# Performance work log

Hardware: AMD Instinct MI355X
Metric: run time of the kernel (lower is better)

## Reference

```python
import jax, jax.numpy as jnp
import numpy as np

NUM_NEURONS = 10000
D = 784
BATCH = 4096


def setup_inputs() -> dict:
    key = jax.random.key(0)
    kx, kw = jax.random.split(key)
    x = jax.random.normal(kx, (BATCH, D), dtype=jnp.float32)
    weights = jax.random.normal(kw, (NUM_NEURONS, D), dtype=jnp.float32)
    return {"x": x, "weights": weights}


def reference(x, weights):
    # SOM BMU lookup: squared distances between each input row and every
    # codebook row, argmin over the codebook, gather the winning neuron.
    # Use |a|^2 + |b|^2 - 2ab to avoid the (B, N, D) broadcast intermediate.
    x = x.reshape(-1, D)  # (B, D)
    x_sq = jnp.sum(x * x, axis=1, keepdims=True)          # (B, 1)
    w_sq = jnp.sum(weights * weights, axis=1)             # (N,)
    cross = x @ weights.T                                 # (B, N) GEMM
    distances = x_sq + w_sq[None, :] - 2.0 * cross        # (B, N)
    bmu_indices = jnp.argmin(distances, axis=1)           # (B,)
    bmu = jnp.take(weights, bmu_indices, axis=0)          # (B, D)
    return bmu
```

## Files before the change

kernel.cpp:

```cpp
#include <hip/hip_runtime.h>
#include <math.h>

#define BATCH 4096
#define D 784
#define N 10000

#define KP 800
#define BK 32
#define KT (KP / BK)
#define BM 128
#define BN 128
#define GXMAX 80
#define NPAD (GXMAX * BN)
#define MARGIN 3.0f

typedef __attribute__((ext_vector_type(8))) short bh8;
typedef __attribute__((ext_vector_type(4))) float fx4;
typedef const __attribute__((address_space(1))) void CGV;
typedef __attribute__((address_space(3))) void LDSV;

static __device__ __forceinline__ unsigned short f2bf(float f) {
    unsigned u = __float_as_uint(f);
    unsigned r = u + 0x7fffu + ((u >> 16) & 1u);
    return (unsigned short)(r >> 16);
}

static __device__ __forceinline__ void top2_insert(float w, int j, float& v0, int& i0,
                                                   float& v1, int& i1) {
    if (w < v0 || (w == v0 && j < i0)) { v1 = v0; i1 = i0; v0 = w; i0 = j; }
    else if (w < v1 || (w == v1 && j < i1)) { v1 = w; i1 = j; }
}

__global__ __launch_bounds__(256) void convert_x_kernel(const float* __restrict__ x,
                                                        unsigned short* __restrict__ xh) {
    int row = blockIdx.x;
    const float4* xr = (const float4*)(x + (size_t)row * D);
    unsigned short* dst = xh + (size_t)row * KP;
    for (int i = threadIdx.x; i < KP / 4; i += 256) {
        int k = i * 4;
        uint2 o;
        if (k < D) {
            float4 v = xr[i];
            o.x = (unsigned)f2bf(v.x) | ((unsigned)f2bf(v.y) << 16);
            o.y = (unsigned)f2bf(v.z) | ((unsigned)f2bf(v.w) << 16);
        } else { o.x = 0u; o.y = 0u; }
        *(uint2*)(dst + k) = o;
    }
}

__global__ __launch_bounds__(256) void convert_w_kernel(const float* __restrict__ w,
                                                        unsigned short* __restrict__ wh,
                                                        float* __restrict__ wsq) {
    int row = blockIdx.x;
    unsigned short* dst = wh + (size_t)row * KP;
    float s = 0.f;
    if (row < N) {
        const float4* wr = (const float4*)(w + (size_t)row * D);
        for (int i = threadIdx.x; i < KP / 4; i += 256) {
            int k = i * 4;
            uint2 o;
            if (k < D) {
                float4 v = wr[i];
                s += v.x * v.x + v.y * v.y + v.z * v.z + v.w * v.w;
                o.x = (unsigned)f2bf(v.x) | ((unsigned)f2bf(v.y) << 16);
                o.y = (unsigned)f2bf(v.z) | ((unsigned)f2bf(v.w) << 16);
            } else { o.x = 0u; o.y = 0u; }
            *(uint2*)(dst + k) = o;
        }
    } else {
        for (int i = threadIdx.x; i < KP / 4; i += 256) {
            uint2 o; o.x = 0u; o.y = 0u;
            *(uint2*)(dst + i * 4) = o;
        }
    }
    __shared__ float sred[4];
    #pragma unroll
    for (int off = 32; off; off >>= 1) s += __shfl_down(s, off);
    if ((threadIdx.x & 63) == 0) sred[threadIdx.x >> 6] = s;
    __syncthreads();
    if (threadIdx.x == 0) {
        float t = sred[0] + sred[1] + sred[2] + sred[3];
        wsq[row] = (row < N) ? t : INFINITY;
    }
}

__global__ __launch_bounds__(256, 4) void dist_mfma_kernel(
    const unsigned short* __restrict__ xh, const unsigned short* __restrict__ wh,
    const float* __restrict__ wsq, float4* __restrict__ partial,
    int gx, int cpb) {
    __shared__ __align__(16) unsigned short As[2][BM * BK];
    __shared__ __align__(16) unsigned short Bs[2][BN * BK];
    __shared__ float4 red[BM][2];

    const int tid = threadIdx.x;
    const int lane = tid & 63;
    const int wid = tid >> 6;
    const int waveM = (wid >> 1) * 64;
    const int waveN = (wid & 1) * 64;

    const int L = blockIdx.x + gx * blockIdx.y;
    const int xcd = L & 7;
    const int s = L >> 3;
    const int bx = s >> 2;
    const int by = xcd * 4 + (s & 3);
    const int rowBase = by * BM;
    const int colBase0 = bx * (cpb * BN);

    const int rr = tid >> 2;
    const int csw = (tid & 3) ^ ((rr >> 1) & 3);
    const unsigned short* aSrc0 = xh + (size_t)(rowBase + rr) * KP + csw * 8;
    const unsigned short* aSrc1 = aSrc0 + (size_t)64 * KP;

    char* ldsA0 = (char*)&As[0][0] + wid * 1024;
    char* ldsA1 = (char*)&As[1][0] + wid * 1024;
    char* ldsB0 = (char*)&Bs[0][0] + wid * 1024;
    char* ldsB1 = (char*)&Bs[1][0] + wid * 1024;

    int offA[4], offB[4];
    #pragma unroll
    for (int m = 0; m < 4; m++) {
        int r = waveM + m * 16 + (lane & 15);
        offA[m] = r * BK + (((lane >> 4) ^ ((r >> 1) & 3)) << 3);
    }
    #pragma unroll
    for (int n = 0; n < 4; n++) {
        int r = waveN + n * 16 + (lane & 15);
        offB[n] = r * BK + (((lane >> 4) ^ ((r >> 1) & 3)) << 3);
    }

    float V0[16], V1[16];
    int I0[16], I1[16];
    #pragma unroll
    for (int q = 0; q < 16; q++) {
        V0[q] = INFINITY; V1[q] = INFINITY;
        I0[q] = 0x7fffffff; I1[q] = 0x7fffffff;
    }

#define STAGE(nb, k0)                                                                  \
    do {                                                                               \
        __builtin_amdgcn_global_load_lds((CGV*)(aSrc0 + (k0)), (LDSV*)(ldsA##nb), 16, 0, 0);        \
        __builtin_amdgcn_global_load_lds((CGV*)(aSrc1 + (k0)), (LDSV*)(ldsA##nb + 4096), 16, 0, 0); \
        __builtin_amdgcn_global_load_lds((CGV*)(bSrc0 + (k0)), (LDSV*)(ldsB##nb), 16, 0, 0);        \
        __builtin_amdgcn_global_load_lds((CGV*)(bSrc1 + (k0)), (LDSV*)(ldsB##nb + 4096), 16, 0, 0); \
    } while (0)

#define COMPUTE(nb)                                                                    \
    do {                                                                               \
        bh8 af[4], bf[4];                                                              \
        _Pragma("unroll")                                                              \
        for (int m = 0; m < 4; m++) af[m] = *(const bh8*)&As[nb][offA[m]];             \
        _Pragma("unroll")                                                              \
        for (int n = 0; n < 4; n++) bf[n] = *(const bh8*)&Bs[nb][offB[n]];             \
        _Pragma("unroll")                                                              \
        for (int m = 0; m < 4; m++)                                                    \
            _Pragma("unroll")                                                          \
            for (int n = 0; n < 4; n++)                                                \
                acc[m][n] = __builtin_amdgcn_mfma_f32_16x16x32_bf16(af[m], bf[n],      \
                                                                    acc[m][n], 0, 0, 0); \
    } while (0)

#define VM0 asm volatile("s_waitcnt vmcnt(0)" ::: "memory")
#define BARR __builtin_amdgcn_s_barrier()

    #pragma unroll 1
    for (int c = 0; c < cpb; ++c) {
        const int colBase = colBase0 + c * BN;
        const unsigned short* bSrc0 = wh + (size_t)(colBase + rr) * KP + csw * 8;
        const unsigned short* bSrc1 = bSrc0 + (size_t)64 * KP;

        fx4 acc[4][4];
        #pragma unroll
        for (int m = 0; m < 4; m++)
            #pragma unroll
            for (int n = 0; n < 4; n++) acc[m][n] = (fx4)0.f;

        STAGE(0, 0);
        VM0; BARR;
        #pragma unroll 1
        for (int t = 0; t < KT - 1; t += 2) {
            STAGE(1, (t + 1) * BK);
            COMPUTE(0);
            VM0; BARR;
            STAGE(0, (t + 2) * BK);
            COMPUTE(1);
            VM0; BARR;
        }
        COMPUTE(0);

        const int cb = colBase + waveN + (lane & 15);
        #pragma unroll
        for (int n = 0; n < 4; n++) {
            const float wq = wsq[cb + n * 16];
            const int ci = cb + n * 16;
            #pragma unroll
            for (int m = 0; m < 4; m++)
                #pragma unroll
                for (int r = 0; r < 4; r++) {
                    float dv = wq - 2.f * acc[m][n][r];
                    top2_insert(dv, ci, V0[m * 4 + r], I0[m * 4 + r],
                                V1[m * 4 + r], I1[m * 4 + r]);
                }
        }
        __syncthreads();
    }

#undef STAGE
#undef COMPUTE
#undef VM0
#undef BARR

    #pragma unroll
    for (int q = 0; q < 16; q++) {
        float v0 = V0[q], v1 = V1[q];
        int i0 = I0[q], i1 = I1[q];
        #pragma unroll
        for (int mask = 1; mask < 16; mask <<= 1) {
            float w0 = __shfl_xor(v0, mask); int j0 = __shfl_xor(i0, mask);
            float w1 = __shfl_xor(v1, mask); int j1 = __shfl_xor(i1, mask);
            top2_insert(w0, j0, v0, i0, v1, i1);
            top2_insert(w1, j1, v0, i0, v1, i1);
        }
        if ((lane & 15) == 0) {
            int m = q >> 2, r = q & 3;
            int row_local = waveM + m * 16 + (lane >> 4) * 4 + r;
            red[row_local][wid & 1] =
                make_float4(v0, __int_as_float(i0), v1, __int_as_float(i1));
        }
    }
    __syncthreads();
    if (tid < BM) {
        float4 pa = red[tid][0], pb = red[tid][1];
        float v0 = pa.x, v1 = pa.z;
        int i0 = __float_as_int(pa.y), i1 = __float_as_int(pa.w);
        top2_insert(pb.x, __float_as_int(pb.y), v0, i0, v1, i1);
        top2_insert(pb.z, __float_as_int(pb.w), v0, i0, v1, i1);
        partial[(size_t)(rowBase + tid) * gx + bx] =
            make_float4(v0, __int_as_float(i0), v1, __int_as_float(i1));
    }
}

__global__ __launch_bounds__(256) void rescore_kernel(const float* __restrict__ x,
                                                      const float* __restrict__ w,
                                                      const float4* __restrict__ partial,
                                                      float* __restrict__ out, int ng) {
    int wid = threadIdx.x >> 6, lane = threadIdx.x & 63;
    int row = blockIdx.x * 4 + wid;
    __shared__ int s_cnt[4];
    __shared__ int s_cand[4][64];

    const float4* part = partial + (size_t)row * ng;

    float bv = INFINITY;
    for (int c = lane; c < ng; c += 64) bv = fminf(bv, part[c].x);
    #pragma unroll
    for (int mask = 1; mask < 64; mask <<= 1) bv = fminf(bv, __shfl_xor(bv, mask));
    float thr = bv + MARGIN;

    if (lane == 0) s_cnt[wid] = 0;
    __syncthreads();
    for (int c = lane; c < ng; c += 64) {
        float4 p = part[c];
        if (p.x <= thr) {
            int pos = atomicAdd(&s_cnt[wid], 1);
            if (pos < 64) s_cand[wid][pos] = __float_as_int(p.y);
        }
        if (p.z <= thr) {
            int pos = atomicAdd(&s_cnt[wid], 1);
            if (pos < 64) s_cand[wid][pos] = __float_as_int(p.w);
        }
    }
    __syncthreads();
    int cnt = s_cnt[wid]; if (cnt > 64) cnt = 64;

    double bd = INFINITY; int bi = 0x7fffffff;
    for (int c = 0; c < cnt; c++) {
        int idx = s_cand[wid][c];
        const float* wr = w + (size_t)idx * D;
        const float* xr = x + (size_t)row * D;
        double s = 0.0;
        for (int d = lane; d < D; d += 64) {
            double wv = (double)wr[d];
            s += wv * (wv - 2.0 * (double)xr[d]);
        }
        #pragma unroll
        for (int mask = 1; mask < 64; mask <<= 1) s += __shfl_xor(s, mask);
        if (s < bd || (s == bd && idx < bi)) { bd = s; bi = idx; }
    }

    const float4* src = (const float4*)(w + (size_t)bi * D);
    float4* dst = (float4*)(out + (size_t)row * D);
    for (int i = lane; i < D / 4; i += 64) dst[i] = src[i];
}

extern "C" void kernel_launch(void* const* d_in, const int* in_sizes, int n_in,
                              void* d_out, int out_size, void* d_ws, size_t ws_size,
                              hipStream_t stream) {
    const float* x = (const float*)d_in[0];
    const float* w = (const float*)d_in[1];
    float* out = (float*)d_out;

    const size_t off_xh = 0;
    const size_t off_wh = off_xh + (size_t)BATCH * KP * 2;
    const size_t off_wsq = off_wh + (size_t)NPAD * KP * 2;
    const size_t off_part = off_wsq + (size_t)NPAD * 4;

    int gx = 80, cpb = 1;
    if (ws_size < off_part + (size_t)BATCH * 80 * 16) { gx = 40; cpb = 2; }
    if (ws_size < off_part + (size_t)BATCH * 40 * 16) { gx = 20; cpb = 4; }

    unsigned short* xh = (unsigned short*)((char*)d_ws + off_xh);
    unsigned short* wh = (unsigned short*)((char*)d_ws + off_wh);
    float* wsq = (float*)((char*)d_ws + off_wsq);
    float4* partial = (float4*)((char*)d_ws + off_part);

    hipLaunchKernelGGL(convert_x_kernel, dim3(BATCH), dim3(256), 0, stream, x, xh);
    hipLaunchKernelGGL(convert_w_kernel, dim3(NPAD), dim3(256), 0, stream, w, wh, wsq);
    hipLaunchKernelGGL(dist_mfma_kernel, dim3(gx, 32), dim3(256), 0, stream,
                       xh, wh, wsq, partial, gx, cpb);
    hipLaunchKernelGGL(rescore_kernel, dim3(BATCH / 4), dim3(256), 0, stream,
                       x, w, partial, out, gx);
}
```

Measured before the change: 570.8 us.

## Triple-buffer LDS tiles with partial vmcnt waits in GEMM main loop

Moves the A/B LDS staging from double to triple buffering. Loads are issued two K-steps ahead, and the loop waits with vmcnt(4) so the previous stage's loads can still be in flight. It also fully unrolls the K loop and cuts each iteration to one barrier instead of waiting on all loads before every compute. In exchange, LDS use rises and the occupancy hint drops from 4 to 3 blocks per CU, which lowers latency hiding across waves.

```diff
diff --git a/kernel.cpp b/kernel.cpp
--- a/kernel.cpp
+++ b/kernel.cpp
@@ -84,12 +84,12 @@
     }
 }
 
-__global__ __launch_bounds__(256, 4) void dist_mfma_kernel(
+__global__ __launch_bounds__(256, 3) void dist_mfma_kernel(
     const unsigned short* __restrict__ xh, const unsigned short* __restrict__ wh,
     const float* __restrict__ wsq, float4* __restrict__ partial,
     int gx, int cpb) {
-    __shared__ __align__(16) unsigned short As[2][BM * BK];
-    __shared__ __align__(16) unsigned short Bs[2][BN * BK];
+    __shared__ __align__(16) unsigned short As[3][BM * BK];
+    __shared__ __align__(16) unsigned short Bs[3][BN * BK];
     __shared__ float4 red[BM][2];
 
     const int tid = threadIdx.x;
@@ -111,21 +111,19 @@
     const unsigned short* aSrc0 = xh + (size_t)(rowBase + rr) * KP + csw * 8;
     const unsigned short* aSrc1 = aSrc0 + (size_t)64 * KP;
 
-    char* ldsA0 = (char*)&As[0][0] + wid * 1024;
-    char* ldsA1 = (char*)&As[1][0] + wid * 1024;
-    char* ldsB0 = (char*)&Bs[0][0] + wid * 1024;
-    char* ldsB1 = (char*)&Bs[1][0] + wid * 1024;
+    char* const ldsA = (char*)&As[0][0] + wid * 1024;
+    char* const ldsB = (char*)&Bs[0][0] + wid * 1024;
 
     int offA[4], offB[4];
     #pragma unroll
     for (int m = 0; m < 4; m++) {
         int r = waveM + m * 16 + (lane & 15);
-        offA[m] = r * BK + (((lane >> 4) ^ ((r >> 1) & 3)) << 3);
+        offA[m] = (r * BK + (((lane >> 4) ^ ((r >> 1) & 3)) << 3)) * 2;
     }
     #pragma unroll
     for (int n = 0; n < 4; n++) {
         int r = waveN + n * 16 + (lane & 15);
-        offB[n] = r * BK + (((lane >> 4) ^ ((r >> 1) & 3)) << 3);
+        offB[n] = (r * BK + (((lane >> 4) ^ ((r >> 1) & 3)) << 3)) * 2;
     }
 
     float V0[16], V1[16];
@@ -136,30 +134,33 @@
         I0[q] = 0x7fffffff; I1[q] = 0x7fffffff;
     }
 
-#define STAGE(nb, k0)                                                                  \
-    do {                                                                               \
-        __builtin_amdgcn_global_load_lds((CGV*)(aSrc0 + (k0)), (LDSV*)(ldsA##nb), 16, 0, 0);        \
-        __builtin_amdgcn_global_load_lds((CGV*)(aSrc1 + (k0)), (LDSV*)(ldsA##nb + 4096), 16, 0, 0); \
-        __builtin_amdgcn_global_load_lds((CGV*)(bSrc0 + (k0)), (LDSV*)(ldsB##nb), 16, 0, 0);        \
-        __builtin_amdgcn_global_load_lds((CGV*)(bSrc1 + (k0)), (LDSV*)(ldsB##nb + 4096), 16, 0, 0); \
+#define STAGE(buf, k0)                                                                     \
+    do {                                                                                   \
+        char* a_ = ldsA + (buf) * 8192;                                                    \
+        char* b_ = ldsB + (buf) * 8192;                                                    \
+        __builtin_amdgcn_global_load_lds((CGV*)(aSrc0 + (k0)), (LDSV*)a_, 16, 0, 0);       \
+        __builtin_amdgcn_global_load_lds((CGV*)(aSrc1 + (k0)), (LDSV*)(a_ + 4096), 16, 0, 0); \
+        __builtin_amdgcn_global_load_lds((CGV*)(bSrc0 + (k0)), (LDSV*)b_, 16, 0, 0);       \
+        __builtin_amdgcn_global_load_lds((CGV*)(bSrc1 + (k0)), (LDSV*)(b_ + 4096), 16, 0, 0); \
     } while (0)
 
-#define COMPUTE(nb)                                                                    \
-    do {                                                                               \
-        bh8 af[4], bf[4];                                                              \
-        _Pragma("unroll")                                                              \
-        for (int m = 0; m < 4; m++) af[m] = *(const bh8*)&As[nb][offA[m]];             \
-        _Pragma("unroll")                                                              \
-        for (int n = 0; n < 4; n++) bf[n] = *(const bh8*)&Bs[nb][offB[n]];             \
-        _Pragma("unroll")                                                              \
-        for (int m = 0; m < 4; m++)                                                    \
-            _Pragma("unroll")                                                          \
-            for (int n = 0; n < 4; n++)                                                \
-                acc[m][n] = __builtin_amdgcn_mfma_f32_16x16x32_bf16(af[m], bf[n],      \
-                                                                    acc[m][n], 0, 0, 0); \
+#define COMPUTE(buf)                                                                       \
+    do {                                                                                   \
+        const char* ab_ = (const char*)&As[0][0] + (buf) * 8192;                           \
+        const char* bb_ = (const char*)&Bs[0][0] + (buf) * 8192;                           \
+        bh8 af[4], bf[4];                                                                  \
+        _Pragma("unroll")                                                                  \
+        for (int m = 0; m < 4; m++) af[m] = *(const bh8*)(ab_ + offA[m]);                  \
+        _Pragma("unroll")                                                                  \
+        for (int n = 0; n < 4; n++) bf[n] = *(const bh8*)(bb_ + offB[n]);                  \
+        _Pragma("unroll")                                                                  \
+        for (int m = 0; m < 4; m++)                                                        \
+            _Pragma("unroll")                                                              \
+            for (int n = 0; n < 4; n++)                                                    \
+                acc[m][n] = __builtin_amdgcn_mfma_f32_16x16x32_bf16(af[m], bf[n],          \
+                                                                    acc[m][n], 0, 0, 0);   \
     } while (0)
 
-#define VM0 asm volatile("s_waitcnt vmcnt(0)" ::: "memory")
 #define BARR __builtin_amdgcn_s_barrier()
 
     #pragma unroll 1
@@ -175,17 +176,16 @@
             for (int n = 0; n < 4; n++) acc[m][n] = (fx4)0.f;
 
         STAGE(0, 0);
-        VM0; BARR;
-        #pragma unroll 1
-        for (int t = 0; t < KT - 1; t += 2) {
-            STAGE(1, (t + 1) * BK);
-            COMPUTE(0);
-            VM0; BARR;
-            STAGE(0, (t + 2) * BK);
-            COMPUTE(1);
-            VM0; BARR;
-        }
-        COMPUTE(0);
+        STAGE(1, BK);
+
+        #pragma unroll
+        for (int t = 0; t < KT; ++t) {
+            if (t < KT - 1) { asm volatile("s_waitcnt vmcnt(4)" ::: "memory"); }
+            else            { asm volatile("s_waitcnt vmcnt(0)" ::: "memory"); }
+            BARR;
+            if (t + 2 < KT) STAGE((t + 2) % 3, (t + 2) * BK);
+            COMPUTE(t % 3);
+        }
 
         const int cb = colBase + waveN + (lane & 15);
         #pragma unroll
@@ -206,7 +206,6 @@
 
 #undef STAGE
 #undef COMPUTE
-#undef VM0
 #undef BARR
 
     #pragma unroll
```

New measurement: 673.2 us. 1.18x slower.

## Add 256x256-tile 512-thread MFMA distance kernel with BK=64 staging

Applied to the files above, without the earlier changes.

Adds a new distance kernel that uses 256x256 output tiles, 8 waves and 128 KB of LDS, staging K in 64-wide chunks with an XOR-swizzled layout and a tail step for the last 32 columns. Each block does the top-2 reduction within each wave and then across waves in LDS. It writes one partial per 256-column tile, so the partial buffer and the rescore pass shrink to 40 candidates per row. The older kernel is kept as a fallback when the workspace is small, with a changed block remap. The larger tiles raise data reuse per LDS load but lower occupancy and grid size, and the kernel needs 128 KB of LDS per block.

```diff
diff --git a/kernel.cpp b/kernel.cpp
--- a/kernel.cpp
+++ b/kernel.cpp
@@ -6,13 +6,18 @@
 #define N 10000
 
 #define KP 800
-#define BK 32
-#define KT (KP / BK)
+#define NPAD 10240
+#define MARGIN 3.0f
+
+#define BM2 256
+#define BN2 256
+#define GX2 40
+#define GY2 16
+
 #define BM 128
 #define BN 128
-#define GXMAX 80
-#define NPAD (GXMAX * BN)
-#define MARGIN 3.0f
+#define BK 32
+#define KT 25
 
 typedef __attribute__((ext_vector_type(8))) short bh8;
 typedef __attribute__((ext_vector_type(4))) float fx4;
@@ -84,12 +89,154 @@
     }
 }
 
-__global__ __launch_bounds__(256, 4) void dist_mfma_kernel(
+__global__ __launch_bounds__(512, 2) void dist_mfma256_kernel(
+    const unsigned short* __restrict__ xh, const unsigned short* __restrict__ wh,
+    const float* __restrict__ wsq, float4* __restrict__ partial) {
+    __shared__ __align__(16) char smem[131072];
+
+    const int tid = threadIdx.x;
+    const int lane = tid & 63;
+    const int wid = tid >> 6;
+    const int waveM = (wid >> 2) * 128;
+    const int wn = wid & 3;
+    const int waveN = wn * 64;
+
+    const int L = blockIdx.x + GX2 * blockIdx.y;
+    const int xcd = L & 7;
+    const int sg = L >> 3;
+    const int bx = sg >> 1;
+    const int by = xcd * 2 + (sg & 1);
+    const int rowBase = by * BM2;
+    const int colBase = bx * BN2;
+
+    const int rr = tid >> 3;
+    const int ps = tid & 7;
+    const int ls = ps ^ (rr & 7);
+    const unsigned short* aS = xh + (size_t)(rowBase + rr) * KP + ls * 8;
+    const unsigned short* bS = wh + (size_t)(colBase + rr) * KP + ls * 8;
+    const int lsc = (ls < 4) ? ls : 3;
+    const unsigned short* aT = xh + (size_t)(rowBase + rr) * KP + 768 + lsc * 8;
+    const unsigned short* bT = wh + (size_t)(colBase + rr) * KP + 768 + lsc * 8;
+
+    char* const ldsA = smem + wid * 1024;
+    char* const ldsB = smem + 32768 + wid * 1024;
+
+    fx4 acc[8][4];
+    #pragma unroll
+    for (int m = 0; m < 8; m++)
+        #pragma unroll
+        for (int n = 0; n < 4; n++) acc[m][n] = (fx4)0.f;
+
+#define STAGE2(buf, k0, Asrc, Bsrc)                                                   \
+    do {                                                                              \
+        char* a_ = ldsA + (buf) * 65536;                                              \
+        char* b_ = ldsB + (buf) * 65536;                                              \
+        _Pragma("unroll")                                                             \
+        for (int j = 0; j < 4; j++) {                                                 \
+            __builtin_amdgcn_global_load_lds((CGV*)(Asrc + (k0) + (size_t)j * 64 * KP), \
+                                             (LDSV*)(a_ + j * 8192), 16, 0, 0);       \
+            __builtin_amdgcn_global_load_lds((CGV*)(Bsrc + (k0) + (size_t)j * 64 * KP), \
+                                             (LDSV*)(b_ + j * 8192), 16, 0, 0);       \
+        }                                                                             \
+    } while (0)
+
+#define KSUB(buf, s)                                                                  \
+    do {                                                                              \
+        const char* A_ = smem + (buf) * 65536;                                        \
+        const char* B_ = smem + (buf) * 65536 + 32768;                                \
+        bh8 af[8], bf[4];                                                             \
+        _Pragma("unroll")                                                             \
+        for (int m = 0; m < 8; m++) {                                                 \
+            int row = waveM + m * 16 + (lane & 15);                                   \
+            int seg = ((s) * 4 + (lane >> 4)) ^ (lane & 7);                           \
+            af[m] = *(const bh8*)(A_ + row * 128 + seg * 16);                         \
+        }                                                                             \
+        _Pragma("unroll")                                                             \
+        for (int n = 0; n < 4; n++) {                                                 \
+            int row = waveN + n * 16 + (lane & 15);                                   \
+            int seg = ((s) * 4 + (lane >> 4)) ^ (lane & 7);                           \
+            bf[n] = *(const bh8*)(B_ + row * 128 + seg * 16);                         \
+        }                                                                             \
+        _Pragma("unroll")                                                             \
+        for (int m = 0; m < 8; m++)                                                   \
+            _Pragma("unroll")                                                         \
+            for (int n = 0; n < 4; n++)                                               \
+                acc[m][n] = __builtin_amdgcn_mfma_f32_16x16x32_bf16(af[m], bf[n],     \
+                                                                    acc[m][n], 0, 0, 0); \
+    } while (0)
+
+    STAGE2(0, 0, aS, bS);
+    asm volatile("s_waitcnt vmcnt(0)" ::: "memory");
+    __builtin_amdgcn_s_barrier();
+
+    #pragma unroll
+    for (int t = 0; t < 12; ++t) {
+        if (t < 11) STAGE2((t + 1) & 1, (t + 1) * 64, aS, bS);
+        else        STAGE2(0, 0, aT, bT);
+        KSUB(t & 1, 0);
+        KSUB(t & 1, 1);
+        asm volatile("s_waitcnt vmcnt(0)" ::: "memory");
+        __builtin_amdgcn_s_barrier();
+    }
+    KSUB(0, 0);
+    __syncthreads();
+
+#undef STAGE2
+#undef KSUB
+
+    float4* red4 = (float4*)smem;
+    const int colT = colBase + waveN + (lane & 15);
+    float wq[4]; int ci[4];
+    #pragma unroll
+    for (int n = 0; n < 4; n++) { ci[n] = colT + n * 16; wq[n] = wsq[ci[n]]; }
+
+    #pragma unroll
+    for (int m = 0; m < 8; m++) {
+        #pragma unroll
+        for (int r = 0; r < 4; r++) {
+            float v0 = INFINITY, v1 = INFINITY;
+            int i0 = 0x7fffffff, i1 = 0x7fffffff;
+            #pragma unroll
+            for (int n = 0; n < 4; n++) {
+                float dv = wq[n] - 2.f * acc[m][n][r];
+                top2_insert(dv, ci[n], v0, i0, v1, i1);
+            }
+            #pragma unroll
+            for (int mask = 1; mask < 16; mask <<= 1) {
+                float w0 = __shfl_xor(v0, mask); int j0 = __shfl_xor(i0, mask);
+                float w1 = __shfl_xor(v1, mask); int j1 = __shfl_xor(i1, mask);
+                top2_insert(w0, j0, v0, i0, v1, i1);
+                top2_insert(w1, j1, v0, i0, v1, i1);
+            }
+            if ((lane & 15) == 0) {
+                int row_local = waveM + m * 16 + (lane >> 4) * 4 + r;
+                red4[row_local * 4 + wn] =
+                    make_float4(v0, __int_as_float(i0), v1, __int_as_float(i1));
+            }
+        }
+    }
+    __syncthreads();
+    if (tid < BM2) {
+        float4 p0 = red4[tid * 4 + 0];
+        float v0 = p0.x, v1 = p0.z;
+        int i0 = __float_as_int(p0.y), i1 = __float_as_int(p0.w);
+        #pragma unroll
+        for (int g = 1; g < 4; g++) {
+            float4 p = red4[tid * 4 + g];
+            top2_insert(p.x, __float_as_int(p.y), v0, i0, v1, i1);
+            top2_insert(p.z, __float_as_int(p.w), v0, i0, v1, i1);
+        }
+        partial[(size_t)(rowBase + tid) * GX2 + bx] =
+            make_float4(v0, __int_as_float(i0), v1, __int_as_float(i1));
+    }
+}
+
+__global__ __launch_bounds__(256, 2) void dist_r3_kernel(
     const unsigned short* __restrict__ xh, const unsigned short* __restrict__ wh,
     const float* __restrict__ wsq, float4* __restrict__ partial,
     int gx, int cpb) {
     __shared__ __align__(16) unsigned short As[2][BM * BK];
-    __shared__ __align__(16) unsigned short Bs[2][BN * BK];
+    __shared__ __align__(16) unsigned short Bs[2][BM * BK];
     __shared__ float4 red[BM][2];
 
     const int tid = threadIdx.x;
@@ -99,10 +246,9 @@
     const int waveN = (wid & 1) * 64;
 
     const int L = blockIdx.x + gx * blockIdx.y;
-    const int xcd = L & 7;
-    const int s = L >> 3;
-    const int bx = s >> 2;
-    const int by = xcd * 4 + (s & 3);
+    const int G = (L & 7) * (gx * 4) + (L >> 3);
+    const int bx = G >> 5;
+    const int by = G & 31;
     const int rowBase = by * BM;
     const int colBase0 = bx * (cpb * BN);
 
@@ -136,31 +282,28 @@
         I0[q] = 0x7fffffff; I1[q] = 0x7fffffff;
     }
 
-#define STAGE(nb, k0)                                                                  \
-    do {                                                                               \
+#define STAGE3(nb, k0)                                                                     \
+    do {                                                                                   \
         __builtin_amdgcn_global_load_lds((CGV*)(aSrc0 + (k0)), (LDSV*)(ldsA##nb), 16, 0, 0);        \
         __builtin_amdgcn_global_load_lds((CGV*)(aSrc1 + (k0)), (LDSV*)(ldsA##nb + 4096), 16, 0, 0); \
         __builtin_amdgcn_global_load_lds((CGV*)(bSrc0 + (k0)), (LDSV*)(ldsB##nb), 16, 0, 0);        \
         __builtin_amdgcn_global_load_lds((CGV*)(bSrc1 + (k0)), (LDSV*)(ldsB##nb + 4096), 16, 0, 0); \
     } while (0)
 
-#define COMPUTE(nb)                                                                    \
-    do {                                                                               \
-        bh8 af[4], bf[4];                                                              \
-        _Pragma("unroll")                                                              \
-        for (int m = 0; m < 4; m++) af[m] = *(const bh8*)&As[nb][offA[m]];             \
-        _Pragma("unroll")                                                              \
-        for (int n = 0; n < 4; n++) bf[n] = *(const bh8*)&Bs[nb][offB[n]];             \
-        _Pragma("unroll")                                                              \
-        for (int m = 0; m < 4; m++)                                                    \
-            _Pragma("unroll")                                                          \
-            for (int n = 0; n < 4; n++)                                                \
-                acc[m][n] = __builtin_amdgcn_mfma_f32_16x16x32_bf16(af[m], bf[n],      \
-                                                                    acc[m][n], 0, 0, 0); \
+#define COMPUTE3(nb)                                                                       \
+    do {                                                                                   \
+        bh8 af[4], bf[4];                                                                  \
+        _Pragma("unroll")                                                                  \
+        for (int m = 0; m < 4; m++) af[m] = *(const bh8*)&As[nb][offA[m]];                 \
+        _Pragma("unroll")                                                                  \
+        for (int n = 0; n < 4; n++) bf[n] = *(const bh8*)&Bs[nb][offB[n]];                 \
+        _Pragma("unroll")                                                                  \
+        for (int m = 0; m < 4; m++)                                                        \
+            _Pragma("unroll")                                                              \
+            for (int n = 0; n < 4; n++)                                                    \
+                acc[m][n] = __builtin_amdgcn_mfma_f32_16x16x32_bf16(af[m], bf[n],          \
+                                                                    acc[m][n], 0, 0, 0);   \
     } while (0)
-
-#define VM0 asm volatile("s_waitcnt vmcnt(0)" ::: "memory")
-#define BARR __builtin_amdgcn_s_barrier()
 
     #pragma unroll 1
     for (int c = 0; c < cpb; ++c) {
@@ -174,18 +317,21 @@
             #pragma unroll
             for (int n = 0; n < 4; n++) acc[m][n] = (fx4)0.f;
 
-        STAGE(0, 0);
-        VM0; BARR;
+        STAGE3(0, 0);
+        asm volatile("s_waitcnt vmcnt(0)" ::: "memory");
+        __builtin_amdgcn_s_barrier();
         #pragma unroll 1
         for (int t = 0; t < KT - 1; t += 2) {
-            STAGE(1, (t + 1) * BK);
-            COMPUTE(0);
-            VM0; BARR;
-            STAGE(0, (t + 2) * BK);
-            COMPUTE(1);
-            VM0; BARR;
-        }
-        COMPUTE(0);
+            STAGE3(1, (t + 1) * BK);
+            COMPUTE3(0);
+            asm volatile("s_waitcnt vmcnt(0)" ::: "memory");
+            __builtin_amdgcn_s_barrier();
+            STAGE3(0, (t + 2) * BK);
+            COMPUTE3(1);
+            asm volatile("s_waitcnt vmcnt(0)" ::: "memory");
+            __builtin_amdgcn_s_barrier();
+        }
+        COMPUTE3(0);
 
         const int cb = colBase + waveN + (lane & 15);
         #pragma unroll
@@ -204,10 +350,8 @@
         __syncthreads();
     }
 
-#undef STAGE
-#undef COMPUTE
-#undef VM0
-#undef BARR
+#undef STAGE3
+#undef COMPUTE3
 
     #pragma unroll
     for (int q = 0; q < 16; q++) {
@@ -303,10 +447,7 @@
     const size_t off_wh = off_xh + (size_t)BATCH * KP * 2;
     const size_t off_wsq = off_wh + (size_t)NPAD * KP * 2;
     const size_t off_part = off_wsq + (size_t)NPAD * 4;
-
-    int gx = 80, cpb = 1;
-    if (ws_size < off_part + (size_t)BATCH * 80 * 16) { gx = 40; cpb = 2; }
-    if (ws_size < off_part + (size_t)BATCH * 40 * 16) { gx = 20; cpb = 4; }
+    const size_t need256 = off_part + (size_t)BATCH * GX2 * 16;
 
     unsigned short* xh = (unsigned short*)((char*)d_ws + off_xh);
     unsigned short* wh = (unsigned short*)((char*)d_ws + off_wh);
@@ -315,8 +456,16 @@
 
     hipLaunchKernelGGL(convert_x_kernel, dim3(BATCH), dim3(256), 0, stream, x, xh);
     hipLaunchKernelGGL(convert_w_kernel, dim3(NPAD), dim3(256), 0, stream, w, wh, wsq);
-    hipLaunchKernelGGL(dist_mfma_kernel, dim3(gx, 32), dim3(256), 0, stream,
-                       xh, wh, wsq, partial, gx, cpb);
-    hipLaunchKernelGGL(rescore_kernel, dim3(BATCH / 4), dim3(256), 0, stream,
-                       x, w, partial, out, gx);
-}
+
+    if (ws_size >= need256) {
+        hipLaunchKernelGGL(dist_mfma256_kernel, dim3(GX2, GY2), dim3(512), 0, stream,
+                           xh, wh, wsq, partial);
+        hipLaunchKernelGGL(rescore_kernel, dim3(BATCH / 4), dim3(256), 0, stream,
+                           x, w, partial, out, GX2);
+    } else {
+        hipLaunchKernelGGL(dist_r3_kernel, dim3(20, 32), dim3(256), 0, stream,
+                           xh, wh, wsq, partial, 20, 4);
+        hipLaunchKernelGGL(rescore_kernel, dim3(BATCH / 4), dim3(256), 0, stream,
+                           x, w, partial, out, 20);
+    }
+}
```

Result: slower. 586.5 us (+2.8%).

## Rewrite distance GEMM with 256x256 tiles, 512 threads and BK=64 pipeline

Applied to the files above, without the earlier changes.

Replaces the 128x128-tile, 256-thread distance kernel with a 256x256-tile, 512-thread kernel that uses a 64-wide K step (12 steps plus a 32-wide tail) and double-buffered 128KB LDS. Larger tiles raise arithmetic intensity and cut global/LDS traffic per MFMA. Partial vmcnt waits and s_setprio are meant to overlap loads with compute. It also drops the ws_size-dependent fallback and uses fixed gx=40. The cost is lower occupancy from heavy LDS and register use, and only 640 blocks to spread across the CUs.

```diff
diff --git a/kernel.cpp b/kernel.cpp
--- a/kernel.cpp
+++ b/kernel.cpp
@@ -6,12 +6,9 @@
 #define N 10000
 
 #define KP 800
-#define BK 32
-#define KT (KP / BK)
-#define BM 128
-#define BN 128
-#define GXMAX 80
-#define NPAD (GXMAX * BN)
+#define NPAD 10240
+#define GX2 40
+#define GY2 16
 #define MARGIN 3.0f
 
 typedef __attribute__((ext_vector_type(8))) short bh8;
@@ -84,157 +81,182 @@
     }
 }
 
-__global__ __launch_bounds__(256, 4) void dist_mfma_kernel(
+__global__ __launch_bounds__(512, 2) void dist_mfma256_kernel(
     const unsigned short* __restrict__ xh, const unsigned short* __restrict__ wh,
-    const float* __restrict__ wsq, float4* __restrict__ partial,
-    int gx, int cpb) {
-    __shared__ __align__(16) unsigned short As[2][BM * BK];
-    __shared__ __align__(16) unsigned short Bs[2][BN * BK];
-    __shared__ float4 red[BM][2];
+    const float* __restrict__ wsq, float4* __restrict__ partial) {
+    __shared__ __align__(16) char smem[131072];
 
     const int tid = threadIdx.x;
     const int lane = tid & 63;
     const int wid = tid >> 6;
-    const int waveM = (wid >> 1) * 64;
-    const int waveN = (wid & 1) * 64;
-
-    const int L = blockIdx.x + gx * blockIdx.y;
+    const int waveM = (wid >> 2) * 128;
+    const int wn = wid & 3;
+    const int waveN = wn * 64;
+
+    const int L = blockIdx.x + GX2 * blockIdx.y;
     const int xcd = L & 7;
-    const int s = L >> 3;
-    const int bx = s >> 2;
-    const int by = xcd * 4 + (s & 3);
-    const int rowBase = by * BM;
-    const int colBase0 = bx * (cpb * BN);
-
-    const int rr = tid >> 2;
-    const int csw = (tid & 3) ^ ((rr >> 1) & 3);
-    const unsigned short* aSrc0 = xh + (size_t)(rowBase + rr) * KP + csw * 8;
-    const unsigned short* aSrc1 = aSrc0 + (size_t)64 * KP;
-
-    char* ldsA0 = (char*)&As[0][0] + wid * 1024;
-    char* ldsA1 = (char*)&As[1][0] + wid * 1024;
-    char* ldsB0 = (char*)&Bs[0][0] + wid * 1024;
-    char* ldsB1 = (char*)&Bs[1][0] + wid * 1024;
-
-    int offA[4], offB[4];
-    #pragma unroll
-    for (int m = 0; m < 4; m++) {
-        int r = waveM + m * 16 + (lane & 15);
-        offA[m] = r * BK + (((lane >> 4) ^ ((r >> 1) & 3)) << 3);
+    const int sg = L >> 3;
+    const int bx = sg >> 1;
+    const int by = xcd * 2 + (sg & 1);
+    const int rowBase = by * 256;
+    const int colBase = bx * 256;
+
+    const int srow = (tid >> 6) * 32 + ((tid >> 3) & 7);
+    const int ls = (tid & 7) ^ ((tid >> 3) & 7);
+    const int lsc = (ls < 4) ? ls : 3;
+
+    const unsigned short* aB[4];
+    const unsigned short* bB[4];
+    const unsigned short* aT[4];
+    const unsigned short* bT[4];
+    #pragma unroll
+    for (int j = 0; j < 4; j++) {
+        aB[j] = xh + (size_t)(rowBase + srow + j * 8) * KP + ls * 8;
+        bB[j] = wh + (size_t)(colBase + srow + j * 8) * KP + ls * 8;
+        aT[j] = xh + (size_t)(rowBase + srow + j * 8) * KP + 768 + lsc * 8;
+        bT[j] = wh + (size_t)(colBase + srow + j * 8) * KP + 768 + lsc * 8;
+    }
+
+    int offA[8][2], offB[4][2];
+    #pragma unroll
+    for (int m = 0; m < 8; m++) {
+        int row = waveM + m * 16 + (lane & 15);
+        #pragma unroll
+        for (int ks = 0; ks < 2; ks++)
+            offA[m][ks] = row * 128 + (((ks * 4 + (lane >> 4)) ^ (row & 7)) << 4);
     }
     #pragma unroll
     for (int n = 0; n < 4; n++) {
-        int r = waveN + n * 16 + (lane & 15);
-        offB[n] = r * BK + (((lane >> 4) ^ ((r >> 1) & 3)) << 3);
-    }
-
-    float V0[16], V1[16];
-    int I0[16], I1[16];
-    #pragma unroll
-    for (int q = 0; q < 16; q++) {
-        V0[q] = INFINITY; V1[q] = INFINITY;
-        I0[q] = 0x7fffffff; I1[q] = 0x7fffffff;
-    }
-
-#define STAGE(nb, k0)                                                                  \
+        int row = waveN + n * 16 + (lane & 15);
+        #pragma unroll
+        for (int ks = 0; ks < 2; ks++)
+            offB[n][ks] = 32768 + row * 128 + (((ks * 4 + (lane >> 4)) ^ (row & 7)) << 4);
+    }
+
+    fx4 acc[8][4];
+    #pragma unroll
+    for (int m = 0; m < 8; m++)
+        #pragma unroll
+        for (int n = 0; n < 4; n++) acc[m][n] = (fx4)0.f;
+
+    char* const ldsAw = smem + wid * 4096;
+    char* const ldsBw = smem + 32768 + wid * 4096;
+
+#define STAGE_N(sel, kt)                                                               \
     do {                                                                               \
-        __builtin_amdgcn_global_load_lds((CGV*)(aSrc0 + (k0)), (LDSV*)(ldsA##nb), 16, 0, 0);        \
-        __builtin_amdgcn_global_load_lds((CGV*)(aSrc1 + (k0)), (LDSV*)(ldsA##nb + 4096), 16, 0, 0); \
-        __builtin_amdgcn_global_load_lds((CGV*)(bSrc0 + (k0)), (LDSV*)(ldsB##nb), 16, 0, 0);        \
-        __builtin_amdgcn_global_load_lds((CGV*)(bSrc1 + (k0)), (LDSV*)(ldsB##nb + 4096), 16, 0, 0); \
+        _Pragma("unroll")                                                              \
+        for (int j = 0; j < 4; j++) {                                                  \
+            __builtin_amdgcn_global_load_lds((CGV*)(aB[j] + (kt) * 64),                \
+                (LDSV*)(ldsAw + (sel) * 65536 + j * 1024), 16, 0, 0);                  \
+            __builtin_amdgcn_global_load_lds((CGV*)(bB[j] + (kt) * 64),                \
+                (LDSV*)(ldsBw + (sel) * 65536 + j * 1024), 16, 0, 0);                  \
+        }                                                                              \
     } while (0)
 
-#define COMPUTE(nb)                                                                    \
+#define STAGE_T(sel)                                                                   \
     do {                                                                               \
-        bh8 af[4], bf[4];                                                              \
         _Pragma("unroll")                                                              \
-        for (int m = 0; m < 4; m++) af[m] = *(const bh8*)&As[nb][offA[m]];             \
-        _Pragma("unroll")                                                              \
-        for (int n = 0; n < 4; n++) bf[n] = *(const bh8*)&Bs[nb][offB[n]];             \
-        _Pragma("unroll")                                                              \
-        for (int m = 0; m < 4; m++)                                                    \
-            _Pragma("unroll")                                                          \
-            for (int n = 0; n < 4; n++)                                                \
-                acc[m][n] = __builtin_amdgcn_mfma_f32_16x16x32_bf16(af[m], bf[n],      \
-                                                                    acc[m][n], 0, 0, 0); \
+        for (int j = 0; j < 4; j++) {                                                  \
+            __builtin_amdgcn_global_load_lds((CGV*)(aT[j]),                            \
+                (LDSV*)(ldsAw + (sel) * 65536 + j * 1024), 16, 0, 0);                  \
+            __builtin_amdgcn_global_load_lds((CGV*)(bT[j]),                            \
+                (LDSV*)(ldsBw + (sel) * 65536 + j * 1024), 16, 0, 0);                  \
+        }                                                                              \
     } while (0)
 
-#define VM0 asm volatile("s_waitcnt vmcnt(0)" ::: "memory")
-#define BARR __builtin_amdgcn_s_barrier()
-
+    STAGE_N(0, 0);
+    asm volatile("s_waitcnt vmcnt(0)" ::: "memory");
+    __builtin_amdgcn_s_barrier();
+
+    int cb = 0;
     #pragma unroll 1
-    for (int c = 0; c < cpb; ++c) {
-        const int colBase = colBase0 + c * BN;
-        const unsigned short* bSrc0 = wh + (size_t)(colBase + rr) * KP + csw * 8;
-        const unsigned short* bSrc1 = bSrc0 + (size_t)64 * KP;
-
-        fx4 acc[4][4];
-        #pragma unroll
-        for (int m = 0; m < 4; m++)
+    for (int t = 0; t < 13; ++t) {
+        if (t < 12) {
+            if (t + 1 < 12) STAGE_N(cb ^ 1, t + 1);
+            else            STAGE_T(cb ^ 1);
+            asm volatile("s_waitcnt vmcnt(8)" ::: "memory");
+        } else {
+            asm volatile("s_waitcnt vmcnt(0)" ::: "memory");
+        }
+        __builtin_amdgcn_s_barrier();
+        __builtin_amdgcn_sched_barrier(0);
+
+        const char* Ab = smem + cb * 65536;
+        const int nks = (t < 12) ? 2 : 1;
+        bh8 bfr[4][2];
+        #pragma unroll
+        for (int n = 0; n < 4; n++)
             #pragma unroll
-            for (int n = 0; n < 4; n++) acc[m][n] = (fx4)0.f;
-
-        STAGE(0, 0);
-        VM0; BARR;
-        #pragma unroll 1
-        for (int t = 0; t < KT - 1; t += 2) {
-            STAGE(1, (t + 1) * BK);
-            COMPUTE(0);
-            VM0; BARR;
-            STAGE(0, (t + 2) * BK);
-            COMPUTE(1);
-            VM0; BARR;
-        }
-        COMPUTE(0);
-
-        const int cb = colBase + waveN + (lane & 15);
-        #pragma unroll
-        for (int n = 0; n < 4; n++) {
-            const float wq = wsq[cb + n * 16];
-            const int ci = cb + n * 16;
+            for (int ks = 0; ks < 2; ks++)
+                if (ks < nks) bfr[n][ks] = *(const bh8*)(Ab + offB[n][ks]);
+        __builtin_amdgcn_s_setprio(1);
+        #pragma unroll
+        for (int m = 0; m < 8; m++) {
+            bh8 a0 = *(const bh8*)(Ab + offA[m][0]);
             #pragma unroll
-            for (int m = 0; m < 4; m++)
+            for (int n = 0; n < 4; n++)
+                acc[m][n] = __builtin_amdgcn_mfma_f32_16x16x32_bf16(a0, bfr[n][0],
+                                                                    acc[m][n], 0, 0, 0);
+            if (nks == 2) {
+                bh8 a1 = *(const bh8*)(Ab + offA[m][1]);
                 #pragma unroll
-                for (int r = 0; r < 4; r++) {
-                    float dv = wq - 2.f * acc[m][n][r];
-                    top2_insert(dv, ci, V0[m * 4 + r], I0[m * 4 + r],
-                                V1[m * 4 + r], I1[m * 4 + r]);
-                }
-        }
-        __syncthreads();
-    }
-
-#undef STAGE
-#undef COMPUTE
-#undef VM0
-#undef BARR
-
-    #pragma unroll
-    for (int q = 0; q < 16; q++) {
-        float v0 = V0[q], v1 = V1[q];
-        int i0 = I0[q], i1 = I1[q];
-        #pragma unroll
-        for (int mask = 1; mask < 16; mask <<= 1) {
-            float w0 = __shfl_xor(v0, mask); int j0 = __shfl_xor(i0, mask);
-            float w1 = __shfl_xor(v1, mask); int j1 = __shfl_xor(i1, mask);
-            top2_insert(w0, j0, v0, i0, v1, i1);
-            top2_insert(w1, j1, v0, i0, v1, i1);
-        }
-        if ((lane & 15) == 0) {
-            int m = q >> 2, r = q & 3;
-            int row_local = waveM + m * 16 + (lane >> 4) * 4 + r;
-            red[row_local][wid & 1] =
-                make_float4(v0, __int_as_float(i0), v1, __int_as_float(i1));
-        }
-    }
-    __syncthreads();
-    if (tid < BM) {
-        float4 pa = red[tid][0], pb = red[tid][1];
-        float v0 = pa.x, v1 = pa.z;
-        int i0 = __float_as_int(pa.y), i1 = __float_as_int(pa.w);
-        top2_insert(pb.x, __float_as_int(pb.y), v0, i0, v1, i1);
-        top2_insert(pb.z, __float_as_int(pb.w), v0, i0, v1, i1);
-        partial[(size_t)(rowBase + tid) * gx + bx] =
+                for (int n = 0; n < 4; n++)
+                    acc[m][n] = __builtin_amdgcn_mfma_f32_16x16x32_bf16(a1, bfr[n][1],
+                                                                        acc[m][n], 0, 0, 0);
+            }
+        }
+        __builtin_amdgcn_s_setprio(0);
+        __builtin_amdgcn_s_barrier();
+        cb ^= 1;
+    }
+#undef STAGE_N
+#undef STAGE_T
+
+    __syncthreads();
+
+    float4* red4 = (float4*)smem;
+    const int colT = colBase + waveN + (lane & 15);
+    float wq[4]; int ci[4];
+    #pragma unroll
+    for (int n = 0; n < 4; n++) { ci[n] = colT + n * 16; wq[n] = wsq[ci[n]]; }
+
+    #pragma unroll
+    for (int m = 0; m < 8; m++) {
+        #pragma unroll
+        for (int r = 0; r < 4; r++) {
+            float v0 = INFINITY, v1 = INFINITY;
+            int i0 = 0x7fffffff, i1 = 0x7fffffff;
+            #pragma unroll
+            for (int n = 0; n < 4; n++) {
+                float dv = wq[n] - 2.f * acc[m][n][r];
+                top2_insert(dv, ci[n], v0, i0, v1, i1);
+            }
+            #pragma unroll
+            for (int mask = 1; mask < 16; mask <<= 1) {
+                float w0 = __shfl_xor(v0, mask); int j0 = __shfl_xor(i0, mask);
+                float w1 = __shfl_xor(v1, mask); int j1 = __shfl_xor(i1, mask);
+                top2_insert(w0, j0, v0, i0, v1, i1);
+                top2_insert(w1, j1, v0, i0, v1, i1);
+            }
+            if ((lane & 15) == 0) {
+                int row_local = waveM + m * 16 + (lane >> 4) * 4 + r;
+                red4[row_local * 4 + wn] =
+                    make_float4(v0, __int_as_float(i0), v1, __int_as_float(i1));
+            }
+        }
+    }
+    __syncthreads();
+    if (tid < 256) {
+        float4 p0 = red4[tid * 4 + 0];
+        float v0 = p0.x, v1 = p0.z;
+        int i0 = __float_as_int(p0.y), i1 = __float_as_int(p0.w);
+        #pragma unroll
+        for (int g = 1; g < 4; g++) {
+            float4 p = red4[tid * 4 + g];
+            top2_insert(p.x, __float_as_int(p.y), v0, i0, v1, i1);
+            top2_insert(p.z, __float_as_int(p.w), v0, i0, v1, i1);
+        }
+        partial[(size_t)(rowBase + tid) * GX2 + bx] =
             make_float4(v0, __int_as_float(i0), v1, __int_as_float(i1));
     }
 }
@@ -304,10 +326,6 @@
     const size_t off_wsq = off_wh + (size_t)NPAD * KP * 2;
     const size_t off_part = off_wsq + (size_t)NPAD * 4;
 
-    int gx = 80, cpb = 1;
-    if (ws_size < off_part + (size_t)BATCH * 80 * 16) { gx = 40; cpb = 2; }
-    if (ws_size < off_part + (size_t)BATCH * 40 * 16) { gx = 20; cpb = 4; }
-
     unsigned short* xh = (unsigned short*)((char*)d_ws + off_xh);
     unsigned short* wh = (unsigned short*)((char*)d_ws + off_wh);
     float* wsq = (float*)((char*)d_ws + off_wsq);
@@ -315,8 +333,8 @@
 
     hipLaunchKernelGGL(convert_x_kernel, dim3(BATCH), dim3(256), 0, stream, x, xh);
     hipLaunchKernelGGL(convert_w_kernel, dim3(NPAD), dim3(256), 0, stream, w, wh, wsq);
-    hipLaunchKernelGGL(dist_mfma_kernel, dim3(gx, 32), dim3(256), 0, stream,
-                       xh, wh, wsq, partial, gx, cpb);
+    hipLaunchKernelGGL(dist_mfma256_kernel, dim3(GX2, GY2), dim3(512), 0, stream,
+                       xh, wh, wsq, partial);
     hipLaunchKernelGGL(rescore_kernel, dim3(BATCH / 4), dim3(256), 0, stream,
-                       x, w, partial, out, gx);
-}
+                       x, w, partial, out, GX2);
+}
```

Measured after the change: 601.6 us. 1.05x slower.
